# Optimization experiments

Measured on AMD Instinct MI355X. Metric: run time of the kernel, lower is better.

Reference implementation:

```python
import jax, jax.numpy as jnp
import numpy as np
from jax import lax

NLAT_IN, NLON_IN = 480, 960
NLAT_OUT, NLON_OUT = 721, 1440
KSIZE = 9      # morlet basis: prod(kernel_shape) = 3*3
NNZ = 20       # sparse quadrature entries per output latitude row
C_IN, C_OUT = 32, 32
BATCH = 1


def setup_inputs() -> dict:
    key = jax.random.key(0)
    k1, k2, k3, k4, k5 = jax.random.split(key, 5)
    x = jax.random.normal(k1, (BATCH, C_IN, NLAT_IN, NLON_IN), dtype=jnp.float32)
    weight = jax.random.normal(k2, (C_OUT, C_IN, KSIZE), dtype=jnp.float32) * 0.05
    # sparse DISCO quadrature values (quadrature weights folded in)
    psi_vals = jax.random.uniform(k3, (KSIZE, NLAT_OUT, NNZ), dtype=jnp.float32) / NNZ
    # geodesic neighborhood: latitude rows within +-2 of output row, small lon offsets
    ho = jnp.arange(NLAT_OUT, dtype=jnp.int32)[:, None]
    psi_hi = jnp.clip(ho + jax.random.randint(k4, (NLAT_OUT, NNZ), -2, 3, dtype=jnp.int32), 0, NLAT_OUT - 1)
    psi_dw = jax.random.randint(k5, (NLAT_OUT, NNZ), -10, 11, dtype=jnp.int32) % NLON_OUT
    return {"x": x, "weight": weight, "psi_vals": psi_vals, "psi_hi": psi_hi, "psi_dw": psi_dw}


def _resample_s2(x, h_out, w_out):
    """Bilinear lat interpolation + periodic linear lon interpolation (ResampleS2)."""
    b, c, h, w = x.shape
    # latitude: both grids are linspace(0, pi, nlat) equiangular
    pos_h = jnp.linspace(0.0, float(h - 1), h_out)
    h0 = jnp.clip(jnp.floor(pos_h).astype(jnp.int32), 0, h - 2)
    fh = (pos_h - h0.astype(jnp.float32)).astype(x.dtype)
    x = x[:, :, h0, :] * (1.0 - fh)[None, None, :, None] + x[:, :, h0 + 1, :] * fh[None, None, :, None]
    # longitude: periodic, lon_j = 2*pi*j/nlon
    pos_w = jnp.arange(w_out, dtype=jnp.float32) * (w / w_out)
    w0 = jnp.floor(pos_w).astype(jnp.int32)
    fw = (pos_w - w0.astype(jnp.float32)).astype(x.dtype)
    w0 = w0 % w
    w1 = (w0 + 1) % w
    return x[..., w0] * (1.0 - fw) + x[..., w1] * fw


def _disco_conv(x, weight, psi_vals, psi_hi, psi_dw):
    """Sparse discrete-continuous spherical conv (gather -> basis weight -> channel mix).
    psi is stored for longitude 0 and applied with a periodic longitude shift."""
    b, c, h, w = x.shape  # [B, Cin, 721, 1440]
    o = weight.shape[0]
    wo = jnp.arange(w, dtype=jnp.int32)

    def body(acc, inp):
        v, hi, dw = inp  # v: [K, Hout], hi/dw: [Hout]
        cols = (dw[:, None] + wo[None, :]) % w          # [Hout, W]
        g = x[:, :, hi[:, None], cols]                  # gather -> [B, Cin, Hout, W]
        weff = jnp.einsum("ock,kh->och", weight, v)     # fold basis into channel mix
        return acc + jnp.einsum("och,bchw->bohw", weff, g), None

    acc0 = jnp.zeros((b, o, h, w), dtype=x.dtype)
    scan_in = (jnp.moveaxis(psi_vals, 2, 0), psi_hi.T, psi_dw.T)  # leading axis NNZ
    acc, _ = lax.scan(body, acc0, scan_in)
    return acc


def reference(x, weight, psi_vals, psi_hi, psi_dw):
    x = _resample_s2(x, NLAT_OUT, NLON_OUT)
    return _disco_conv(x, weight, psi_vals, psi_hi, psi_dw)
```

## Files before the change

### kernel.cpp

```cpp
#include <hip/hip_runtime.h>
#include <hip/hip_bf16.h>

#define NLAT_IN  480
#define NLON_IN  960
#define NLAT_OUT 721
#define NLON_OUT 1440
#define KSIZE    9
#define NNZ      20
#define CH       32

typedef __bf16 bf16x8 __attribute__((ext_vector_type(8)));
typedef float  f32x4  __attribute__((ext_vector_type(4)));
typedef unsigned u32x4 __attribute__((ext_vector_type(4)));

__device__ __forceinline__ unsigned short f2bf(float f) {
    unsigned u = __float_as_uint(f);
    u += 0x7fffu + ((u >> 16) & 1u);
    return (unsigned short)(u >> 16);
}

#define W_TILE   180
#define IN_LD4   31
#define LDS_PITCH 129
#define NBLK_WEFF 902
#define NBLK_RES  (8 * NLAT_OUT)

__global__ __launch_bounds__(256) void pre_kernel(
        const float* __restrict__ x,
        const float* __restrict__ weight,
        const float* __restrict__ psi_vals,
        unsigned short* __restrict__ xr,
        unsigned short* __restrict__ weff) {
    __shared__ float smem[KSIZE * CH * CH];

    const int bid = blockIdx.x;
    const int t   = threadIdx.x;

    if (bid < NBLK_WEFF) {
        float* wl = smem;
        for (int i = 0; i < 9; ++i) {
            int lin = i * 256 + t;
            if (lin < KSIZE * CH * CH / 4) {
                f32x4 v = *(const f32x4*)(weight + lin * 4);
                float vv[4] = {v.x, v.y, v.z, v.w};
#pragma unroll
                for (int q = 0; q < 4; ++q) {
                    int l4 = lin * 4 + q;
                    int k  = l4 % KSIZE;
                    int occ = l4 / KSIZE;
                    wl[k * (CH * CH) + occ] = vv[q];
                }
            }
        }
        __syncthreads();

        int hnz = bid * 16 + (t >> 4);
        int cp  = t & 15;
        if (hnz >= NLAT_OUT * NNZ) return;

        float p[KSIZE];
#pragma unroll
        for (int k = 0; k < KSIZE; ++k)
            p[k] = psi_vals[(size_t)k * (NLAT_OUT * NNZ) + hnz];

        unsigned* outp = (unsigned*)weff + (size_t)hnz * (CH * CH / 2) + cp;
#pragma unroll 4
        for (int oc = 0; oc < CH; ++oc) {
            float a0 = 0.f, a1 = 0.f;
            const float* wb = wl + oc * CH + cp * 2;
#pragma unroll
            for (int k = 0; k < KSIZE; ++k) {
                a0 += wb[k * (CH * CH)]     * p[k];
                a1 += wb[k * (CH * CH) + 1] * p[k];
            }
            outp[oc * 16] = (unsigned)f2bf(a0) | ((unsigned)f2bf(a1) << 16);
        }
        return;
    }

    float* ld = smem;
    int bid2 = bid - NBLK_WEFF;
    int bx = bid2 & 7;
    int h  = bid2 >> 3;
    int wb = bx * W_TILE;
    int base_in = bx * (W_TILE * 2 / 3);

    float pos_h = (float)h * (479.0f / 720.0f);
    int h0 = (int)floorf(pos_h);
    if (h0 < 0) h0 = 0;
    if (h0 > NLAT_IN - 2) h0 = NLAT_IN - 2;
    float fh = pos_h - (float)h0;

    for (int i = 0; i < 8; ++i) {
        int lin = i * 256 + t;
        if (lin < 2 * CH * IN_LD4) {
            int r   = lin / (CH * IN_LD4);
            int rem = lin - r * (CH * IN_LD4);
            int c   = rem / IN_LD4;
            int j   = rem - c * IN_LD4;
            int src = base_in + 4 * j;
            if (src >= NLON_IN) src -= NLON_IN;
            f32x4 v = *(const f32x4*)(x + ((size_t)c * NLAT_IN + h0 + r) * NLON_IN + src);
            float* dst = ld + (r * CH + c) * LDS_PITCH + 4 * j;
            dst[0] = v.x; dst[1] = v.y; dst[2] = v.z; dst[3] = v.w;
        }
    }
    __syncthreads();

    float ifh = 1.0f - fh;
    for (int i = 0; i < 3; ++i) {
        int d = i * 256 + t;
        if (d >= W_TILE * (CH / 8)) break;
        int w_l = d >> 2;
        int cg  = d & 3;
        int w = wb + w_l;
        float pos_w = (float)w * ((float)NLON_IN / (float)NLON_OUT);
        int w0 = (int)floorf(pos_w);
        float fw = pos_w - (float)w0;
        int wl0 = w0 - base_in;
        float ifw = 1.0f - fw;

        unsigned rr[4];
#pragma unroll
        for (int j = 0; j < 4; ++j) {
            int c = cg * 8 + j * 2;
            const float* r0 = ld + c * LDS_PITCH + wl0;
            const float* r1 = r0 + CH * LDS_PITCH;
            float v0 = ifh * (ifw * r0[0] + fw * r0[1]) + fh * (ifw * r1[0] + fw * r1[1]);
            const float* q0 = r0 + LDS_PITCH;
            const float* q1 = r1 + LDS_PITCH;
            float v1 = ifh * (ifw * q0[0] + fw * q0[1]) + fh * (ifw * q1[0] + fw * q1[1]);
            rr[j] = (unsigned)f2bf(v0) | ((unsigned)f2bf(v1) << 16);
        }
        u32x4 uv; uv[0] = rr[0]; uv[1] = rr[1]; uv[2] = rr[2]; uv[3] = rr[3];
        *(u32x4*)((unsigned*)xr + ((size_t)h * NLON_OUT + w) * (CH / 2) + cg * 4) = uv;
    }
}

#define ST_ROWS 8
#define ST_COLS 80
#define WC      48
#define HBLK4   181
#define NWBLK   (NLON_OUT / WC)
#define NPAIRD  (HBLK4 * NWBLK)
#define PER_XCD ((NPAIRD + 7) / 8)

__global__ __launch_bounds__(256, 4) void disco_kernel(
        const unsigned short* __restrict__ xr,
        const unsigned short* __restrict__ weff,
        const int* __restrict__ psi_hi,
        const int* __restrict__ psi_dw,
        float* __restrict__ out) {
    __shared__ unsigned short st[ST_ROWS * ST_COLS * CH];

    int bid = blockIdx.x;
    int xcd = bid & 7;
    int p   = xcd * PER_XCD + (bid >> 3);
    if (p >= NPAIRD) return;
    int hblk = p / NWBLK;
    int wblk = p - hblk * NWBLK;
    int h0        = hblk * 4;
    int wbase_blk = wblk * WC;

    int wave = threadIdx.x >> 6;
    int lane = threadIdx.x & 63;
    int l15  = lane & 15;
    int quad = lane >> 4;
    int c0   = quad * 8;

    int  h  = h0 + wave;
    bool hv = (h < NLAT_OUT);

    int swz = ((lane >> 2) << 5) + (((lane & 3) ^ ((lane >> 3) & 3)) << 3);

    int cstart = wbase_blk - 16;
    if (cstart < 0) cstart += NLON_OUT;
    for (int i = wave; i < ST_ROWS * (ST_COLS / 16); i += 4) {
        int r  = i / 5;
        int ck = i - r * 5;
        int gh = h0 - 2 + r;
        gh = gh < 0 ? 0 : (gh > NLAT_OUT - 1 ? NLAT_OUT - 1 : gh);
        int gc = cstart + ck * 16;
        if (gc >= NLON_OUT) gc -= NLON_OUT;
        const unsigned short* gp = xr + ((size_t)gh * NLON_OUT + gc) * CH + swz;
        unsigned short* lp = st + (r * ST_COLS + ck * 16) * CH;
        __builtin_amdgcn_global_load_lds(
            (const __attribute__((address_space(1))) void*)gp,
            (__attribute__((address_space(3))) void*)lp, 16, 0, 0);
    }

    const unsigned short* weff_h = weff + (size_t)h * (NNZ * CH * CH);
    const int* hip_ = psi_hi + h * NNZ;
    const int* dwp  = psi_dw + h * NNZ;

    bf16x8 pa0[4], pa1[4];
    int phi[4], pdw[4];
    if (hv) {
#pragma unroll
        for (int q = 0; q < 4; ++q) {
            const unsigned short* wp = weff_h + q * (CH * CH);
            pa0[q] = *(const bf16x8*)(wp + l15 * CH + c0);
            pa1[q] = *(const bf16x8*)(wp + (16 + l15) * CH + c0);
            phi[q] = hip_[q];
            pdw[q] = dwp[q];
        }
    }
    __syncthreads();

    if (hv) {
        f32x4 acc[2][3] = {};
        int wcol0 = 16 + l15;

#pragma unroll
        for (int nz = 0; nz < NNZ; ++nz) {
            const int sl = nz & 3;
            bf16x8 a0 = pa0[sl];
            bf16x8 a1 = pa1[sl];
            int hi = phi[sl];
            int dw = pdw[sl];
            if (nz + 4 < NNZ) {
                const unsigned short* wp = weff_h + (nz + 4) * (CH * CH);
                pa0[sl] = *(const bf16x8*)(wp + l15 * CH + c0);
                pa1[sl] = *(const bf16x8*)(wp + (16 + l15) * CH + c0);
                phi[sl] = hip_[nz + 4];
                pdw[sl] = dwp[nz + 4];
            }
            int shift = dw > 720 ? dw - NLON_OUT : dw;
            int rloc  = hi - h0 + 2;
            int cbase = wcol0 + shift;
            int sel   = ((((cbase >> 1) & 3) ^ quad) << 3);
            const unsigned short* bp =
                st + (size_t)rloc * (ST_COLS * CH) + cbase * CH + sel;
#pragma unroll
            for (int s = 0; s < 3; ++s) {
                bf16x8 b = *(const bf16x8*)(bp + s * 16 * CH);
                acc[0][s] = __builtin_amdgcn_mfma_f32_16x16x32_bf16(a0, b, acc[0][s], 0, 0, 0);
                acc[1][s] = __builtin_amdgcn_mfma_f32_16x16x32_bf16(a1, b, acc[1][s], 0, 0, 0);
            }
        }

#pragma unroll
        for (int hh = 0; hh < 2; ++hh)
#pragma unroll
            for (int s = 0; s < 3; ++s)
#pragma unroll
                for (int r = 0; r < 4; ++r) {
                    int oc = hh * 16 + quad * 4 + r;
                    int w  = wbase_blk + s * 16 + l15;
                    out[((size_t)oc * NLAT_OUT + h) * NLON_OUT + w] = acc[hh][s][r];
                }
    }
}

extern "C" void kernel_launch(void* const* d_in, const int* in_sizes, int n_in,
                              void* d_out, int out_size, void* d_ws, size_t ws_size,
                              hipStream_t stream) {
    const float* x        = (const float*)d_in[0];
    const float* weight   = (const float*)d_in[1];
    const float* psi_vals = (const float*)d_in[2];
    const int*   psi_hi   = (const int*)d_in[3];
    const int*   psi_dw   = (const int*)d_in[4];
    float* out = (float*)d_out;

    unsigned short* xr = (unsigned short*)d_ws;
    unsigned short* wf = (unsigned short*)((char*)d_ws + (size_t)NLAT_OUT * NLON_OUT * CH * 2);

    {
        pre_kernel<<<NBLK_WEFF + NBLK_RES, 256, 0, stream>>>(x, weight, psi_vals, xr, wf);
    }
    {
        disco_kernel<<<8 * PER_XCD, 256, 0, stream>>>(xr, wf, psi_hi, psi_dw, out);
    }
}
```

Measured before the change: 304.3 us.

## Make disco kernel persistent over latitude chunks with double-buffered LDS tiles

Each disco block now has 512 threads covering a 96-column tile and loops over 3 consecutive 4-row latitude groups. It double-buffers the LDS stencil tile, issuing async global-to-LDS loads for the next group while MFMAs run on the current one. The aim is to hide tile-load latency and amortize setup over more work per block, and wider tiles reduce the share of halo columns loaded. In exchange, LDS use doubles and grows per block, which lowers occupancy, the grid becomes much smaller with a tail from the uneven chunk split, and the XCD-aware block remapping is dropped.

```diff
diff --git a/kernel.cpp b/kernel.cpp
--- a/kernel.cpp
+++ b/kernel.cpp
@@ -138,117 +138,140 @@
 }
 
 #define ST_ROWS 8
-#define ST_COLS 80
-#define WC      48
-#define HBLK4   181
-#define NWBLK   (NLON_OUT / WC)
-#define NPAIRD  (HBLK4 * NWBLK)
-#define PER_XCD ((NPAIRD + 7) / 8)
-
-__global__ __launch_bounds__(256, 4) void disco_kernel(
+#define ST_COLS 128
+#define TILE_E  (ST_ROWS * ST_COLS * CH)
+#define CHUNK_H 3
+#define NHBLK   181
+#define NCHUNK  ((NHBLK + CHUNK_H - 1) / CHUNK_H)
+#define NWBLK   15
+#define NBLK_D  (NCHUNK * NWBLK)
+
+__global__ __launch_bounds__(512, 2) void disco_kernel(
         const unsigned short* __restrict__ xr,
         const unsigned short* __restrict__ weff,
         const int* __restrict__ psi_hi,
         const int* __restrict__ psi_dw,
         float* __restrict__ out) {
-    __shared__ unsigned short st[ST_ROWS * ST_COLS * CH];
-
-    int bid = blockIdx.x;
-    int xcd = bid & 7;
-    int p   = xcd * PER_XCD + (bid >> 3);
-    if (p >= NPAIRD) return;
-    int hblk = p / NWBLK;
-    int wblk = p - hblk * NWBLK;
-    int h0        = hblk * 4;
-    int wbase_blk = wblk * WC;
-
-    int wave = threadIdx.x >> 6;
-    int lane = threadIdx.x & 63;
-    int l15  = lane & 15;
-    int quad = lane >> 4;
-    int c0   = quad * 8;
-
-    int  h  = h0 + wave;
-    bool hv = (h < NLAT_OUT);
-
-    int swz = ((lane >> 2) << 5) + (((lane & 3) ^ ((lane >> 3) & 3)) << 3);
+    __shared__ unsigned short st[2 * TILE_E];
+
+    const int bid   = blockIdx.x;
+    const int wblk  = bid % NWBLK;
+    const int chunk = bid / NWBLK;
+    const int hb0   = chunk * CHUNK_H;
+    const int nt    = (NHBLK - hb0) < CHUNK_H ? (NHBLK - hb0) : CHUNK_H;
+    const int wbase_blk = wblk * 96;
+
+    const int wave = threadIdx.x >> 6;
+    const int lane = threadIdx.x & 63;
+    const int l15  = lane & 15;
+    const int quad = lane >> 4;
+    const int c0   = quad * 8;
+    const int jh   = wave >> 1;
+    const int wq   = wave & 1;
+
+    const int swz = ((lane >> 2) << 5) + (((lane & 3) ^ ((lane >> 3) & 3)) << 3);
 
     int cstart = wbase_blk - 16;
     if (cstart < 0) cstart += NLON_OUT;
-    for (int i = wave; i < ST_ROWS * (ST_COLS / 16); i += 4) {
-        int r  = i / 5;
-        int ck = i - r * 5;
-        int gh = h0 - 2 + r;
-        gh = gh < 0 ? 0 : (gh > NLAT_OUT - 1 ? NLAT_OUT - 1 : gh);
-        int gc = cstart + ck * 16;
-        if (gc >= NLON_OUT) gc -= NLON_OUT;
-        const unsigned short* gp = xr + ((size_t)gh * NLON_OUT + gc) * CH + swz;
-        unsigned short* lp = st + (r * ST_COLS + ck * 16) * CH;
-        __builtin_amdgcn_global_load_lds(
-            (const __attribute__((address_space(1))) void*)gp,
-            (__attribute__((address_space(3))) void*)lp, 16, 0, 0);
-    }
-
-    const unsigned short* weff_h = weff + (size_t)h * (NNZ * CH * CH);
-    const int* hip_ = psi_hi + h * NNZ;
-    const int* dwp  = psi_dw + h * NNZ;
-
-    bf16x8 pa0[4], pa1[4];
-    int phi[4], pdw[4];
-    if (hv) {
-#pragma unroll
-        for (int q = 0; q < 4; ++q) {
-            const unsigned short* wp = weff_h + q * (CH * CH);
-            pa0[q] = *(const bf16x8*)(wp + l15 * CH + c0);
-            pa1[q] = *(const bf16x8*)(wp + (16 + l15) * CH + c0);
-            phi[q] = hip_[q];
-            pdw[q] = dwp[q];
+
+    {
+        const int h0 = hb0 * 4;
+        for (int i = wave; i < ST_ROWS * (ST_COLS / 16); i += 8) {
+            int r = i >> 3, ck = i & 7;
+            int gh = h0 - 2 + r;
+            gh = gh < 0 ? 0 : (gh > NLAT_OUT - 1 ? NLAT_OUT - 1 : gh);
+            int gc = cstart + ck * 16;
+            if (gc >= NLON_OUT) gc -= NLON_OUT;
+            const unsigned short* gp = xr + ((size_t)gh * NLON_OUT + gc) * CH + swz;
+            unsigned short* lp = st + (r * ST_COLS + ck * 16) * CH;
+            __builtin_amdgcn_global_load_lds(
+                (const __attribute__((address_space(1))) void*)gp,
+                (__attribute__((address_space(3))) void*)lp, 16, 0, 0);
         }
     }
     __syncthreads();
 
-    if (hv) {
-        f32x4 acc[2][3] = {};
-        int wcol0 = 16 + l15;
-
-#pragma unroll
-        for (int nz = 0; nz < NNZ; ++nz) {
-            const int sl = nz & 3;
-            bf16x8 a0 = pa0[sl];
-            bf16x8 a1 = pa1[sl];
-            int hi = phi[sl];
-            int dw = pdw[sl];
-            if (nz + 4 < NNZ) {
-                const unsigned short* wp = weff_h + (nz + 4) * (CH * CH);
-                pa0[sl] = *(const bf16x8*)(wp + l15 * CH + c0);
-                pa1[sl] = *(const bf16x8*)(wp + (16 + l15) * CH + c0);
-                phi[sl] = hip_[nz + 4];
-                pdw[sl] = dwp[nz + 4];
-            }
-            int shift = dw > 720 ? dw - NLON_OUT : dw;
-            int rloc  = hi - h0 + 2;
-            int cbase = wcol0 + shift;
-            int sel   = ((((cbase >> 1) & 3) ^ quad) << 3);
-            const unsigned short* bp =
-                st + (size_t)rloc * (ST_COLS * CH) + cbase * CH + sel;
-#pragma unroll
-            for (int s = 0; s < 3; ++s) {
-                bf16x8 b = *(const bf16x8*)(bp + s * 16 * CH);
-                acc[0][s] = __builtin_amdgcn_mfma_f32_16x16x32_bf16(a0, b, acc[0][s], 0, 0, 0);
-                acc[1][s] = __builtin_amdgcn_mfma_f32_16x16x32_bf16(a1, b, acc[1][s], 0, 0, 0);
-            }
-        }
-
-#pragma unroll
-        for (int hh = 0; hh < 2; ++hh)
-#pragma unroll
-            for (int s = 0; s < 3; ++s)
-#pragma unroll
-                for (int r = 0; r < 4; ++r) {
-                    int oc = hh * 16 + quad * 4 + r;
-                    int w  = wbase_blk + s * 16 + l15;
-                    out[((size_t)oc * NLAT_OUT + h) * NLON_OUT + w] = acc[hh][s][r];
+    for (int t = 0; t < nt; ++t) {
+        if (t + 1 < nt) {
+            const int h0n = (hb0 + t + 1) * 4;
+            unsigned short* bufn = st + ((t + 1) & 1) * TILE_E;
+            for (int i = wave; i < ST_ROWS * (ST_COLS / 16); i += 8) {
+                int r = i >> 3, ck = i & 7;
+                int gh = h0n - 2 + r;
+                gh = gh < 0 ? 0 : (gh > NLAT_OUT - 1 ? NLAT_OUT - 1 : gh);
+                int gc = cstart + ck * 16;
+                if (gc >= NLON_OUT) gc -= NLON_OUT;
+                const unsigned short* gp = xr + ((size_t)gh * NLON_OUT + gc) * CH + swz;
+                unsigned short* lp = bufn + (r * ST_COLS + ck * 16) * CH;
+                __builtin_amdgcn_global_load_lds(
+                    (const __attribute__((address_space(1))) void*)gp,
+                    (__attribute__((address_space(3))) void*)lp, 16, 0, 0);
+            }
+        }
+
+        const int h0 = (hb0 + t) * 4;
+        const int h  = h0 + jh;
+        const unsigned short* bt = st + (t & 1) * TILE_E;
+
+        if (h < NLAT_OUT) {
+            const unsigned short* weff_h = weff + (size_t)h * (NNZ * CH * CH);
+            const int* hip_ = psi_hi + h * NNZ;
+            const int* dwp  = psi_dw + h * NNZ;
+
+            bf16x8 pa0[4], pa1[4];
+            int phi[4], pdw[4];
+#pragma unroll
+            for (int q = 0; q < 4; ++q) {
+                const unsigned short* wp = weff_h + q * (CH * CH);
+                pa0[q] = *(const bf16x8*)(wp + l15 * CH + c0);
+                pa1[q] = *(const bf16x8*)(wp + (16 + l15) * CH + c0);
+                phi[q] = hip_[q];
+                pdw[q] = dwp[q];
+            }
+
+            f32x4 acc[2][3] = {};
+            const int wcol0 = 16 + wq * 48 + l15;
+
+#pragma unroll
+            for (int nz = 0; nz < NNZ; ++nz) {
+                const int sl = nz & 3;
+                bf16x8 a0 = pa0[sl];
+                bf16x8 a1 = pa1[sl];
+                int hi = phi[sl];
+                int dw = pdw[sl];
+                if (nz + 4 < NNZ) {
+                    const unsigned short* wp = weff_h + (nz + 4) * (CH * CH);
+                    pa0[sl] = *(const bf16x8*)(wp + l15 * CH + c0);
+                    pa1[sl] = *(const bf16x8*)(wp + (16 + l15) * CH + c0);
+                    phi[sl] = hip_[nz + 4];
+                    pdw[sl] = dwp[nz + 4];
                 }
+                int shift = dw > 720 ? dw - NLON_OUT : dw;
+                int rloc  = hi - h0 + 2;
+                int cbase = wcol0 + shift;
+                int sel   = ((((cbase >> 1) & 3) ^ quad) << 3);
+                const unsigned short* bp =
+                    bt + (size_t)rloc * (ST_COLS * CH) + cbase * CH + sel;
+#pragma unroll
+                for (int s = 0; s < 3; ++s) {
+                    bf16x8 b = *(const bf16x8*)(bp + s * 16 * CH);
+                    acc[0][s] = __builtin_amdgcn_mfma_f32_16x16x32_bf16(a0, b, acc[0][s], 0, 0, 0);
+                    acc[1][s] = __builtin_amdgcn_mfma_f32_16x16x32_bf16(a1, b, acc[1][s], 0, 0, 0);
+                }
+            }
+
+#pragma unroll
+            for (int hh = 0; hh < 2; ++hh)
+#pragma unroll
+                for (int s = 0; s < 3; ++s)
+#pragma unroll
+                    for (int r = 0; r < 4; ++r) {
+                        int oc = hh * 16 + quad * 4 + r;
+                        int w  = wbase_blk + wq * 48 + s * 16 + l15;
+                        out[((size_t)oc * NLAT_OUT + h) * NLON_OUT + w] = acc[hh][s][r];
+                    }
+        }
+        __syncthreads();
     }
 }
 
@@ -269,6 +292,6 @@
         pre_kernel<<<NBLK_WEFF + NBLK_RES, 256, 0, stream>>>(x, weight, psi_vals, xr, wf);
     }
     {
-        disco_kernel<<<8 * PER_XCD, 256, 0, stream>>>(xr, wf, psi_hi, psi_dw, out);
-    }
-}
+        disco_kernel<<<NBLK_D, 512, 0, stream>>>(xr, wf, psi_hi, psi_dw, out);
+    }
+}
```

Result: slower. 347.6 us (+14.2%).

## Drop LDS staging in disco kernel; gather B operands directly from global/L2

Applied to the files above, without the earlier changes.

Removes the shared-memory tile staging (global_load_lds plus barrier) and has each wave independently read its bf16 input columns straight from global memory, relying on L1/L2 for the heavy reuse across neighboring rows and offsets. Work is redistributed so each wave owns one (row, 48-column strip) task, with wrap-around handled per column, and prefetch depth for weights drops from 4 to 2 to allow higher occupancy (launch bounds 5). This saves LDS traffic and synchronization but trades it for many more uncoalesced-ish global loads that depend on cache hit rates.

```diff
diff --git a/kernel.cpp b/kernel.cpp
--- a/kernel.cpp
+++ b/kernel.cpp
@@ -137,119 +137,87 @@
     }
 }
 
-#define ST_ROWS 8
-#define ST_COLS 80
-#define WC      48
-#define HBLK4   181
-#define NWBLK   (NLON_OUT / WC)
-#define NPAIRD  (HBLK4 * NWBLK)
-#define PER_XCD ((NPAIRD + 7) / 8)
-
-__global__ __launch_bounds__(256, 4) void disco_kernel(
+#define WSTRIP   30
+#define NTASK    (NLAT_OUT * WSTRIP)
+#define NBLK_D   ((NTASK + 3) / 4)
+#define PER_XCD2 (NBLK_D / 8)
+
+__global__ __launch_bounds__(256, 5) void disco_kernel(
         const unsigned short* __restrict__ xr,
         const unsigned short* __restrict__ weff,
         const int* __restrict__ psi_hi,
         const int* __restrict__ psi_dw,
         float* __restrict__ out) {
-    __shared__ unsigned short st[ST_ROWS * ST_COLS * CH];
-
-    int bid = blockIdx.x;
-    int xcd = bid & 7;
-    int p   = xcd * PER_XCD + (bid >> 3);
-    if (p >= NPAIRD) return;
-    int hblk = p / NWBLK;
-    int wblk = p - hblk * NWBLK;
-    int h0        = hblk * 4;
-    int wbase_blk = wblk * WC;
-
-    int wave = threadIdx.x >> 6;
-    int lane = threadIdx.x & 63;
-    int l15  = lane & 15;
-    int quad = lane >> 4;
-    int c0   = quad * 8;
-
-    int  h  = h0 + wave;
-    bool hv = (h < NLAT_OUT);
-
-    int swz = ((lane >> 2) << 5) + (((lane & 3) ^ ((lane >> 3) & 3)) << 3);
-
-    int cstart = wbase_blk - 16;
-    if (cstart < 0) cstart += NLON_OUT;
-    for (int i = wave; i < ST_ROWS * (ST_COLS / 16); i += 4) {
-        int r  = i / 5;
-        int ck = i - r * 5;
-        int gh = h0 - 2 + r;
-        gh = gh < 0 ? 0 : (gh > NLAT_OUT - 1 ? NLAT_OUT - 1 : gh);
-        int gc = cstart + ck * 16;
-        if (gc >= NLON_OUT) gc -= NLON_OUT;
-        const unsigned short* gp = xr + ((size_t)gh * NLON_OUT + gc) * CH + swz;
-        unsigned short* lp = st + (r * ST_COLS + ck * 16) * CH;
-        __builtin_amdgcn_global_load_lds(
-            (const __attribute__((address_space(1))) void*)gp,
-            (__attribute__((address_space(3))) void*)lp, 16, 0, 0);
-    }
+    const int bid = blockIdx.x;
+    const int bp  = (bid & 7) * PER_XCD2 + (bid >> 3);
+    const int task = bp * 4 + (int)(threadIdx.x >> 6);
+    if (task >= NTASK) return;
+
+    const int h     = task / WSTRIP;
+    const int strip = task - h * WSTRIP;
+    const int wbase = strip * 48;
+
+    const int lane = threadIdx.x & 63;
+    const int l15  = lane & 15;
+    const int quad = lane >> 4;
+    const int c0   = quad * 8;
 
     const unsigned short* weff_h = weff + (size_t)h * (NNZ * CH * CH);
     const int* hip_ = psi_hi + h * NNZ;
     const int* dwp  = psi_dw + h * NNZ;
 
-    bf16x8 pa0[4], pa1[4];
-    int phi[4], pdw[4];
-    if (hv) {
-#pragma unroll
-        for (int q = 0; q < 4; ++q) {
-            const unsigned short* wp = weff_h + q * (CH * CH);
-            pa0[q] = *(const bf16x8*)(wp + l15 * CH + c0);
-            pa1[q] = *(const bf16x8*)(wp + (16 + l15) * CH + c0);
-            phi[q] = hip_[q];
-            pdw[q] = dwp[q];
-        }
-    }
-    __syncthreads();
-
-    if (hv) {
-        f32x4 acc[2][3] = {};
-        int wcol0 = 16 + l15;
-
-#pragma unroll
-        for (int nz = 0; nz < NNZ; ++nz) {
-            const int sl = nz & 3;
-            bf16x8 a0 = pa0[sl];
-            bf16x8 a1 = pa1[sl];
-            int hi = phi[sl];
-            int dw = pdw[sl];
-            if (nz + 4 < NNZ) {
-                const unsigned short* wp = weff_h + (nz + 4) * (CH * CH);
-                pa0[sl] = *(const bf16x8*)(wp + l15 * CH + c0);
-                pa1[sl] = *(const bf16x8*)(wp + (16 + l15) * CH + c0);
-                phi[sl] = hip_[nz + 4];
-                pdw[sl] = dwp[nz + 4];
+    bf16x8 pa0[2], pa1[2];
+    int phi[2], pdw[2];
+#pragma unroll
+    for (int q = 0; q < 2; ++q) {
+        const unsigned short* wp = weff_h + q * (CH * CH);
+        pa0[q] = *(const bf16x8*)(wp + l15 * CH + c0);
+        pa1[q] = *(const bf16x8*)(wp + (16 + l15) * CH + c0);
+        phi[q] = hip_[q];
+        pdw[q] = dwp[q];
+    }
+
+    f32x4 acc[2][3] = {};
+    const int cb0 = wbase + l15;
+
+#pragma unroll
+    for (int nz = 0; nz < NNZ; ++nz) {
+        const int sl = nz & 1;
+        bf16x8 a0 = pa0[sl];
+        bf16x8 a1 = pa1[sl];
+        int hi = phi[sl];
+        int dw = pdw[sl];
+        if (nz + 2 < NNZ) {
+            const unsigned short* wp = weff_h + (nz + 2) * (CH * CH);
+            pa0[sl] = *(const bf16x8*)(wp + l15 * CH + c0);
+            pa1[sl] = *(const bf16x8*)(wp + (16 + l15) * CH + c0);
+            phi[sl] = hip_[nz + 2];
+            pdw[sl] = dwp[nz + 2];
+        }
+        int shift = dw > 720 ? dw - NLON_OUT : dw;
+        int cb = cb0 + shift;
+        if (cb < 0) cb += NLON_OUT;
+        const unsigned short* xrow = xr + (size_t)hi * (NLON_OUT * CH);
+#pragma unroll
+        for (int s = 0; s < 3; ++s) {
+            int cc = cb + s * 16;
+            cc = cc >= NLON_OUT ? cc - NLON_OUT : cc;
+            bf16x8 b = *(const bf16x8*)(xrow + (size_t)cc * CH + c0);
+            acc[0][s] = __builtin_amdgcn_mfma_f32_16x16x32_bf16(a0, b, acc[0][s], 0, 0, 0);
+            acc[1][s] = __builtin_amdgcn_mfma_f32_16x16x32_bf16(a1, b, acc[1][s], 0, 0, 0);
+        }
+    }
+
+#pragma unroll
+    for (int hh = 0; hh < 2; ++hh)
+#pragma unroll
+        for (int s = 0; s < 3; ++s)
+#pragma unroll
+            for (int r = 0; r < 4; ++r) {
+                int oc = hh * 16 + quad * 4 + r;
+                int w  = wbase + s * 16 + l15;
+                out[((size_t)oc * NLAT_OUT + h) * NLON_OUT + w] = acc[hh][s][r];
             }
-            int shift = dw > 720 ? dw - NLON_OUT : dw;
-            int rloc  = hi - h0 + 2;
-            int cbase = wcol0 + shift;
-            int sel   = ((((cbase >> 1) & 3) ^ quad) << 3);
-            const unsigned short* bp =
-                st + (size_t)rloc * (ST_COLS * CH) + cbase * CH + sel;
-#pragma unroll
-            for (int s = 0; s < 3; ++s) {
-                bf16x8 b = *(const bf16x8*)(bp + s * 16 * CH);
-                acc[0][s] = __builtin_amdgcn_mfma_f32_16x16x32_bf16(a0, b, acc[0][s], 0, 0, 0);
-                acc[1][s] = __builtin_amdgcn_mfma_f32_16x16x32_bf16(a1, b, acc[1][s], 0, 0, 0);
-            }
-        }
-
-#pragma unroll
-        for (int hh = 0; hh < 2; ++hh)
-#pragma unroll
-            for (int s = 0; s < 3; ++s)
-#pragma unroll
-                for (int r = 0; r < 4; ++r) {
-                    int oc = hh * 16 + quad * 4 + r;
-                    int w  = wbase_blk + s * 16 + l15;
-                    out[((size_t)oc * NLAT_OUT + h) * NLON_OUT + w] = acc[hh][s][r];
-                }
-    }
 }
 
 extern "C" void kernel_launch(void* const* d_in, const int* in_sizes, int n_in,
@@ -269,6 +237,6 @@
         pre_kernel<<<NBLK_WEFF + NBLK_RES, 256, 0, stream>>>(x, weight, psi_vals, xr, wf);
     }
     {
-        disco_kernel<<<8 * PER_XCD, 256, 0, stream>>>(xr, wf, psi_hi, psi_dw, out);
-    }
-}
+        disco_kernel<<<NBLK_D, 256, 0, stream>>>(xr, wf, psi_hi, psi_dw, out);
+    }
+}
```

Result: slower. 373.8 us (+22.8%).
